# Kernel optimization log

Measured on AMD Instinct MI355X. Metric: run time of the kernel, lower is better.

## Reference

```python
import jax, jax.numpy as jnp
import numpy as np

EMBED = 1024
HEADS = 16

def setup_inputs() -> dict:
    key = jax.random.key(0)
    k1, k2, k3, k4, k5 = jax.random.split(key, 5)
    x = jax.random.normal(k1, (2, 2048, EMBED), dtype=jnp.float32)
    s = 1.0 / np.sqrt(EMBED)
    W_atten = jax.random.normal(k2, (EMBED, 3 * EMBED), dtype=jnp.float32) * s
    b_atten = jax.random.normal(k3, (3 * EMBED,), dtype=jnp.float32) * 0.01
    W_proj = jax.random.normal(k4, (EMBED, EMBED), dtype=jnp.float32) * s
    b_proj = jax.random.normal(k5, (EMBED,), dtype=jnp.float32) * 0.01
    return {"x": x, "W_atten": W_atten, "b_atten": b_atten, "W_proj": W_proj, "b_proj": b_proj}

def reference(x, W_atten, b_atten, W_proj, b_proj):
    B, T, C = x.shape
    H = HEADS
    hs = C // H
    qkv = x @ W_atten + b_atten  # [B,T,3C]
    # NOTE: original splits as k, q, v (k first)
    k, q, v = jnp.split(qkv, 3, axis=2)
    k = k.reshape(B, T, H, hs).transpose(0, 2, 1, 3)  # [B,H,T,hs]
    q = q.reshape(B, T, H, hs).transpose(0, 2, 1, 3)
    v = v.reshape(B, T, H, hs).transpose(0, 2, 1, 3)
    scores = jnp.einsum('bhqd,bhkd->bhqk', q, k) / jnp.sqrt(jnp.float32(hs))
    causal = jnp.tril(jnp.ones((T, T), dtype=bool))
    scores = jnp.where(causal[None, None, :, :], scores, jnp.float32(-jnp.inf))
    att = jax.nn.softmax(scores, axis=-1)
    out = jnp.einsum('bhqk,bhkd->bhqd', att, v)  # [B,H,T,hs]
    out = out.transpose(0, 2, 1, 3).reshape(B, T, C)
    return out @ W_proj + b_proj
```

## Files before the change

kernel.cpp:

```cpp
#include <hip/hip_runtime.h>

typedef unsigned short u16;
typedef unsigned int u32;
typedef __bf16 bf16;
typedef bf16 bf16x8 __attribute__((ext_vector_type(8)));
typedef float f32x4 __attribute__((ext_vector_type(4)));
typedef u32 u32x4 __attribute__((ext_vector_type(4)));
typedef u16 u16x4 __attribute__((ext_vector_type(4)));

#define EMBED 1024
#define HEADS 16
#define HS 64
#define BATCH 2
#define SEQ 2048
#define M_TOT (BATCH * SEQ)
#define N_QKV (3 * EMBED)
#define KDIM  EMBED

#define CSCALE 0.18033688011112042f
#define MREF (64.0f * CSCALE)

__device__ __forceinline__ u16 f2bf(float f) {
  u32 u = __builtin_bit_cast(u32, f);
  u32 r = u + 0x7fffu + ((u >> 16) & 1u);
  return (u16)(r >> 16);
}
__device__ __forceinline__ float bf2f(u16 h) {
  return __builtin_bit_cast(float, (u32)h << 16);
}
__device__ __forceinline__ bf16x8 frag16(const u16* p) {
  return __builtin_bit_cast(bf16x8, *(const u32x4*)p);
}
__device__ __forceinline__ bf16x8 frag16u(const u32* p) {
  return __builtin_bit_cast(bf16x8, *(const u32x4*)p);
}
__device__ __forceinline__ float cl(float v) {
  return fminf(fmaxf(v, -3.0e4f), 3.0e4f);
}
__device__ __forceinline__ u32 pk2bf(float lo, float hi) {
  const u32 ul = __builtin_bit_cast(u32, lo) + 0x8000u;
  const u32 uh = __builtin_bit_cast(u32, hi) + 0x8000u;
  return (ul >> 16) | (uh & 0xFFFF0000u);
}

typedef __attribute__((address_space(1))) void gvoid;
typedef __attribute__((address_space(3))) void lvoid;
__device__ __forceinline__ void glds16(const u16* g, u16* l) {
  __builtin_amdgcn_global_load_lds((gvoid*)g, (lvoid*)l, 16, 0, 0);
}

__global__ __launch_bounds__(256) void convert_kernel(
    const float* __restrict__ in, u16* __restrict__ out, int n4) {
  const int i = blockIdx.x * 256 + threadIdx.x;
  if (i < n4) {
    f32x4 v = *(const f32x4*)(in + (size_t)i * 4);
    u16x4 pk;
#pragma unroll
    for (int j = 0; j < 4; j++) pk[j] = f2bf(v[j]);
    *(u16x4*)(out + (size_t)i * 4) = pk;
  }
}

__global__ __launch_bounds__(256) void transpose_conv_kernel(
    const float* __restrict__ in, u16* __restrict__ out, int R, int C) {
  __shared__ u16 tile[32][33];
  const int c0 = blockIdx.x * 32;
  const int r0 = blockIdx.y * 32;
  const int tx = threadIdx.x;
  const int ty = threadIdx.y;
#pragma unroll
  for (int i = 0; i < 32; i += 8)
    tile[ty + i][tx] = f2bf(in[(size_t)(r0 + ty + i) * C + c0 + tx]);
  __syncthreads();
#pragma unroll
  for (int i = 0; i < 32; i += 8)
    out[(size_t)(c0 + ty + i) * R + r0 + tx] = tile[tx][ty + i];
}

__global__ __launch_bounds__(256) void gemm_qkv_kernel(
    const u16* __restrict__ A, const u16* __restrict__ wt,
    const u16* __restrict__ bias, u16* __restrict__ kq, u16* __restrict__ vt) {
  __shared__ u16 As[128 * 32];
  __shared__ u16 Bs[128 * 32];
  const int tid = threadIdx.x;
  const int lane = tid & 63;
  const int wave = tid >> 6;
  const int quad = lane >> 4;
  const int l16 = lane & 15;
  const int wr = wave >> 1;
  const int wc = wave & 1;
  const int m0 = blockIdx.y * 128;
  const int n0 = blockIdx.x * 128;

  f32x4 acc[4][4] = {};
  const int grow = tid >> 2;
  const int gcol = (tid & 3) * 8;

  for (int k0 = 0; k0 < KDIM; k0 += 32) {
    __syncthreads();
    glds16(A + (size_t)(m0 + grow) * KDIM + k0 + gcol, As + tid * 8);
    glds16(A + (size_t)(m0 + grow + 64) * KDIM + k0 + gcol, As + 2048 + tid * 8);
    glds16(wt + (size_t)(n0 + grow) * KDIM + k0 + gcol, Bs + tid * 8);
    glds16(wt + (size_t)(n0 + grow + 64) * KDIM + k0 + gcol, Bs + 2048 + tid * 8);
    __syncthreads();

    bf16x8 af[4], bfr[4];
#pragma unroll
    for (int i = 0; i < 4; i++) {
      af[i]  = frag16(As + (wr * 64 + i * 16 + l16) * 32 + quad * 8);
      bfr[i] = frag16(Bs + (wc * 64 + i * 16 + l16) * 32 + quad * 8);
    }
#pragma unroll
    for (int mi = 0; mi < 4; mi++)
#pragma unroll
      for (int ni = 0; ni < 4; ni++)
        acc[mi][ni] = __builtin_amdgcn_mfma_f32_16x16x32_bf16(
            af[mi], bfr[ni], acc[mi][ni], 0, 0, 0);
  }

#pragma unroll
  for (int ni = 0; ni < 4; ni++) {
    const int n = n0 + wc * 64 + ni * 16 + l16;
    const float bv = bf2f(bias[n]);
    if (n < 2 * EMBED) {
#pragma unroll
      for (int mi = 0; mi < 4; mi++)
#pragma unroll
        for (int r = 0; r < 4; r++) {
          const int m = m0 + wr * 64 + mi * 16 + quad * 4 + r;
          kq[(size_t)m * 2048 + n] = f2bf(cl(acc[mi][ni][r] + bv));
        }
    } else {
      const int hd = n - 2 * EMBED;
      const int h2 = hd >> 6;
      const int dc2 = (hd >> 4) & 3;
#pragma unroll
      for (int mi = 0; mi < 4; mi++) {
        const int mbase = m0 + wr * 64 + mi * 16 + quad * 4;
        const int bqi = mbase >> 11;
        const int t0 = mbase & 2047;
        const int kt2 = t0 >> 6;
        const int kc2 = (t0 >> 5) & 1;
        const int qt2 = (t0 >> 3) & 3;
        const int e0 = t0 & 7;
        u16x4 pk;
#pragma unroll
        for (int r = 0; r < 4; r++) pk[r] = f2bf(cl(acc[mi][ni][r] + bv));
        const size_t idx =
            ((((size_t)(bqi * 16 + h2) * 32 + kt2) * 2 + kc2) * 4 + dc2) * 512 +
            (qt2 * 16 + l16) * 8 + e0;
        *(u16x4*)(vt + idx) = pk;
      }
    }
  }
}

__global__ __launch_bounds__(128) void gemm_proj_kernel(
    const u16* __restrict__ A, const u16* __restrict__ wt,
    const u16* __restrict__ bias, float* __restrict__ out) {
  __shared__ u16 As[128 * 32];
  __shared__ u16 Bs[64 * 32];
  const int tid = threadIdx.x;
  const int lane = tid & 63;
  const int wave = tid >> 6;
  const int quad = lane >> 4;
  const int l16 = lane & 15;
  const int m0 = blockIdx.y * 128;
  const int n0 = blockIdx.x * 64;

  f32x4 acc[4][4] = {};
  const int grow = tid >> 2;
  const int gcol = (tid & 3) * 8;

  for (int k0 = 0; k0 < KDIM; k0 += 32) {
    __syncthreads();
#pragma unroll
    for (int p = 0; p < 4; p++)
      glds16(A + (size_t)(m0 + p * 32 + grow) * KDIM + k0 + gcol,
             As + p * 1024 + tid * 8);
#pragma unroll
    for (int p = 0; p < 2; p++)
      glds16(wt + (size_t)(n0 + p * 32 + grow) * KDIM + k0 + gcol,
             Bs + p * 1024 + tid * 8);
    __syncthreads();

    bf16x8 af[4], bfr[4];
#pragma unroll
    for (int i = 0; i < 4; i++) {
      af[i]  = frag16(As + (wave * 64 + i * 16 + l16) * 32 + quad * 8);
      bfr[i] = frag16(Bs + (i * 16 + l16) * 32 + quad * 8);
    }
#pragma unroll
    for (int mi = 0; mi < 4; mi++)
#pragma unroll
      for (int ni = 0; ni < 4; ni++)
        acc[mi][ni] = __builtin_amdgcn_mfma_f32_16x16x32_bf16(
            af[mi], bfr[ni], acc[mi][ni], 0, 0, 0);
  }

#pragma unroll
  for (int ni = 0; ni < 4; ni++) {
    const int n = n0 + ni * 16 + l16;
    const float bv = bf2f(bias[n]);
#pragma unroll
    for (int mi = 0; mi < 4; mi++)
#pragma unroll
      for (int r = 0; r < 4; r++) {
        const int m = m0 + wave * 64 + mi * 16 + quad * 4 + r;
        out[(size_t)m * EMBED + n] = cl(acc[mi][ni][r] + bv);
      }
  }
}

__global__ __launch_bounds__(64) void attn_kernel(
    const u16* __restrict__ kq, const u16* __restrict__ vt,
    u16* __restrict__ att) {
  __shared__ u16 Ks[2][64 * 64];
  __shared__ u32 Ps32[2][16 * 32];

  const int tid = threadIdx.x;
  const int quad = (tid >> 4) & 3;
  const int l16 = tid & 15;

  const int bh = blockIdx.x;
  const int qt32 = 63 - (int)blockIdx.y;
  const int q0 = qt32 * 32;
  const int bq = bh >> 4;
  const int h = bh & 15;

  int qg[2];
  bf16x8 bq0[2], bq1[2];
#pragma unroll
  for (int g = 0; g < 2; g++) {
    qg[g] = q0 + g * 16 + l16;
    const size_t qrow = (size_t)(bq * SEQ + qg[g]) * 2048 + EMBED + h * HS;
    bq0[g] = frag16(kq + qrow + quad * 8);
    bq1[g] = frag16(kq + qrow + 32 + quad * 8);
  }

  const u16* kb = kq + (size_t)bq * SEQ * 2048 + h * HS;
  const u16* vb2 = vt + (size_t)(bq * 16 + h) * 32 * 4096;
  const int psw32 = (l16 & 7) << 2;

  const int sw = quad ^ (l16 & 7);

  float lsum[2] = {0.0f, 0.0f};
  f32x4 o[2][4] = {};

  const int nkt = (qt32 >> 1) + 1;
#pragma unroll
  for (int p = 0; p < 8; p++) {
    const int row = p * 8 + (tid >> 3);
    const int sgc = (tid & 7) ^ (row & 7);
    glds16(kb + (size_t)row * 2048 + sgc * 8, Ks[0] + row * 64 + (tid & 7) * 8);
  }

  for (int kt = 0; kt < nkt; kt++) {
    const int k0 = kt * 64;
    __syncthreads();
    if (kt + 1 < nkt) {
      const int kn = k0 + 64;
      u16* dst = Ks[(kt + 1) & 1];
#pragma unroll
      for (int p = 0; p < 8; p++) {
        const int row = p * 8 + (tid >> 3);
        const int sgc = (tid & 7) ^ (row & 7);
        glds16(kb + (size_t)(kn + row) * 2048 + sgc * 8, dst + row * 64 + (tid & 7) * 8);
      }
    }
    const u16* KsB = Ks[kt & 1];

    bf16x8 va[2][4];
#pragma unroll
    for (int kc = 0; kc < 2; kc++)
#pragma unroll
      for (int dc = 0; dc < 4; dc++)
        va[kc][dc] = frag16(vb2 + (size_t)kt * 4096 +
                            ((kc * 4 + dc) * 64 + quad * 16 + l16) * 8);

    f32x4 st[2][4] = {};
    __builtin_amdgcn_s_setprio(1);
#pragma unroll
    for (int sub = 0; sub < 4; sub++) {
      const u16* kr = KsB + (sub * 16 + l16) * 64;
      const bf16x8 ka0 = frag16(kr + sw * 8);
      const bf16x8 ka1 = frag16(kr + (sw ^ 4) * 8);
#pragma unroll
      for (int g = 0; g < 2; g++) {
        st[g][sub] = __builtin_amdgcn_mfma_f32_16x16x32_bf16(
            ka0, bq0[g], st[g][sub], 0, 0, 0);
        st[g][sub] = __builtin_amdgcn_mfma_f32_16x16x32_bf16(
            ka1, bq1[g], st[g][sub], 0, 0, 0);
      }
    }
    __builtin_amdgcn_s_setprio(0);

    const bool diag = (kt == nkt - 1);
#pragma unroll
    for (int g = 0; g < 2; g++) {
      float p[4][4];
      if (diag) {
#pragma unroll
        for (int sub = 0; sub < 4; sub++)
#pragma unroll
          for (int r = 0; r < 4; r++) {
            const int key = k0 + sub * 16 + quad * 4 + r;
            const float e = __builtin_amdgcn_exp2f(st[g][sub][r] * CSCALE - MREF);
            p[sub][r] = (key <= qg[g]) ? e : 0.0f;
            lsum[g] += p[sub][r];
          }
      } else {
#pragma unroll
        for (int sub = 0; sub < 4; sub++)
#pragma unroll
          for (int r = 0; r < 4; r++) {
            p[sub][r] = __builtin_amdgcn_exp2f(st[g][sub][r] * CSCALE - MREF);
            lsum[g] += p[sub][r];
          }
      }
      u32* pw = Ps32[g];
#pragma unroll
      for (int sub = 0; sub < 4; sub++)
#pragma unroll
        for (int rp = 0; rp < 2; rp++)
          pw[l16 * 32 + ((sub * 8 + quad * 2 + rp) ^ psw32)] =
              pk2bf(p[sub][2 * rp], p[sub][2 * rp + 1]);
    }

#pragma unroll
    for (int g = 0; g < 2; g++) {
      u32* pw = Ps32[g];
#pragma unroll
      for (int kc = 0; kc < 2; kc++) {
        bf16x8 pb = frag16u(pw + l16 * 32 + ((kc * 16 + quad * 4) ^ psw32));
        __builtin_amdgcn_s_setprio(1);
#pragma unroll
        for (int dc = 0; dc < 4; dc++)
          o[g][dc] = __builtin_amdgcn_mfma_f32_16x16x32_bf16(
              va[kc][dc], pb, o[g][dc], 0, 0, 0);
        __builtin_amdgcn_s_setprio(0);
      }
    }
  }

#pragma unroll
  for (int g = 0; g < 2; g++) {
    float ls = lsum[g];
    ls += __shfl_xor(ls, 16);
    ls += __shfl_xor(ls, 32);
    const float inv = 1.0f / ls;
    const size_t obase = (size_t)(bq * SEQ + qg[g]) * EMBED + h * HS;
#pragma unroll
    for (int dc = 0; dc < 4; dc++) {
      u16 sv[4];
#pragma unroll
      for (int r = 0; r < 4; r++) sv[r] = f2bf(cl(o[g][dc][r] * inv));
      *(u32*)(att + obase + dc * 16 + quad * 4) = (u32)sv[0] | ((u32)sv[1] << 16);
      *(u32*)(att + obase + dc * 16 + quad * 4 + 2) = (u32)sv[2] | ((u32)sv[3] << 16);
    }
  }
}

extern "C" void kernel_launch(void* const* d_in, const int* in_sizes, int n_in,
                              void* d_out, int out_size, void* d_ws,
                              size_t ws_size, hipStream_t stream) {
  const float* x       = (const float*)d_in[0];
  const float* W_atten = (const float*)d_in[1];
  const float* b_atten = (const float*)d_in[2];
  const float* W_proj  = (const float*)d_in[3];
  const float* b_proj  = (const float*)d_in[4];

  u16* wt_a = (u16*)d_ws;
  u16* wt_p = wt_a + (size_t)N_QKV * EMBED;
  u16* ba   = wt_p + (size_t)EMBED * EMBED;
  u16* bp   = ba + N_QKV;
  u16* xb   = bp + EMBED;
  u16* kq   = xb + (size_t)M_TOT * KDIM;
  u16* vt   = kq + (size_t)M_TOT * 2048;
  u16* attb = xb;

  convert_kernel<<<(M_TOT * KDIM / 4 + 255) / 256, 256, 0, stream>>>(
      x, xb, M_TOT * KDIM / 4);
  convert_kernel<<<(N_QKV / 4 + 255) / 256, 256, 0, stream>>>(b_atten, ba, N_QKV / 4);
  convert_kernel<<<(EMBED / 4 + 255) / 256, 256, 0, stream>>>(b_proj, bp, EMBED / 4);
  transpose_conv_kernel<<<dim3(N_QKV / 32, EMBED / 32), dim3(32, 8), 0, stream>>>(
      W_atten, wt_a, EMBED, N_QKV);
  transpose_conv_kernel<<<dim3(EMBED / 32, EMBED / 32), dim3(32, 8), 0, stream>>>(
      W_proj, wt_p, EMBED, EMBED);
  gemm_qkv_kernel<<<dim3(N_QKV / 128, M_TOT / 128), 256, 0, stream>>>(
      xb, wt_a, ba, kq, vt);
  attn_kernel<<<dim3(BATCH * HEADS, SEQ / 32), 64, 0, stream>>>(kq, vt, attb);
  gemm_proj_kernel<<<dim3(EMBED / 64, M_TOT / 128), 128, 0, stream>>>(
      attb, wt_p, bp, (float*)d_out);
}
```

Measured before the change: 191.3 us.

## Pair causal query tiles per block and compute row sums via MFMA

The attention kernel now runs two independent waves per block. One wave takes a long causal query tile and the other a short one (yy and 63-yy), so every block gets the same amount of work and the grid is halved. Each wave has its own K and P shared buffers and waits on vmcnt instead of a block barrier. The softmax denominator, previously summed per element with shuffles, now comes from an extra MFMA of P against a ones vector. This adds shared memory per block and one MFMA per chunk, and drops the scalar adds and cross-lane reductions.

```diff
diff --git a/kernel.cpp b/kernel.cpp
--- a/kernel.cpp
+++ b/kernel.cpp
@@ -212,18 +212,21 @@
   }
 }
 
-__global__ __launch_bounds__(64) void attn_kernel(
+__global__ __launch_bounds__(128) void attn_kernel(
     const u16* __restrict__ kq, const u16* __restrict__ vt,
     u16* __restrict__ att) {
-  __shared__ u16 Ks[2][64 * 64];
-  __shared__ u32 Ps32[2][16 * 32];
+  __shared__ u16 Ks[2][2][64 * 64];
+  __shared__ u32 Ps32[2][2][16 * 32];
 
   const int tid = threadIdx.x;
-  const int quad = (tid >> 4) & 3;
-  const int l16 = tid & 15;
+  const int lane = tid & 63;
+  const int wave = tid >> 6;
+  const int quad = (lane >> 4) & 3;
+  const int l16 = lane & 15;
 
   const int bh = blockIdx.x;
-  const int qt32 = 63 - (int)blockIdx.y;
+  const int yy = (int)blockIdx.y;
+  const int qt32 = wave ? yy : (63 - yy);
   const int q0 = qt32 * 32;
   const int bq = bh >> 4;
   const int h = bh & 15;
@@ -241,34 +244,40 @@
   const u16* kb = kq + (size_t)bq * SEQ * 2048 + h * HS;
   const u16* vb2 = vt + (size_t)(bq * 16 + h) * 32 * 4096;
   const int psw32 = (l16 & 7) << 2;
-
   const int sw = quad ^ (l16 & 7);
 
-  float lsum[2] = {0.0f, 0.0f};
+  u32x4 onesu;
+#pragma unroll
+  for (int j = 0; j < 4; j++) onesu[j] = 0x3F803F80u;
+  const bf16x8 ones8 = __builtin_bit_cast(bf16x8, onesu);
+
   f32x4 o[2][4] = {};
+  f32x4 o4[2] = {};
 
   const int nkt = (qt32 >> 1) + 1;
+  u16* ksw = (u16*)Ks[wave];
+
 #pragma unroll
   for (int p = 0; p < 8; p++) {
-    const int row = p * 8 + (tid >> 3);
-    const int sgc = (tid & 7) ^ (row & 7);
-    glds16(kb + (size_t)row * 2048 + sgc * 8, Ks[0] + row * 64 + (tid & 7) * 8);
+    const int row = p * 8 + (lane >> 3);
+    const int sgc = (lane & 7) ^ (row & 7);
+    glds16(kb + (size_t)row * 2048 + sgc * 8, ksw + row * 64 + (lane & 7) * 8);
   }
 
   for (int kt = 0; kt < nkt; kt++) {
     const int k0 = kt * 64;
-    __syncthreads();
+    asm volatile("s_waitcnt vmcnt(0)" ::: "memory");
     if (kt + 1 < nkt) {
       const int kn = k0 + 64;
-      u16* dst = Ks[(kt + 1) & 1];
+      u16* dst = ksw + ((kt + 1) & 1) * (64 * 64);
 #pragma unroll
       for (int p = 0; p < 8; p++) {
-        const int row = p * 8 + (tid >> 3);
-        const int sgc = (tid & 7) ^ (row & 7);
-        glds16(kb + (size_t)(kn + row) * 2048 + sgc * 8, dst + row * 64 + (tid & 7) * 8);
-      }
-    }
-    const u16* KsB = Ks[kt & 1];
+        const int row = p * 8 + (lane >> 3);
+        const int sgc = (lane & 7) ^ (row & 7);
+        glds16(kb + (size_t)(kn + row) * 2048 + sgc * 8, dst + row * 64 + (lane & 7) * 8);
+      }
+    }
+    const u16* KsB = ksw + (kt & 1) * (64 * 64);
 
     bf16x8 va[2][4];
 #pragma unroll
@@ -307,18 +316,15 @@
             const int key = k0 + sub * 16 + quad * 4 + r;
             const float e = __builtin_amdgcn_exp2f(st[g][sub][r] * CSCALE - MREF);
             p[sub][r] = (key <= qg[g]) ? e : 0.0f;
-            lsum[g] += p[sub][r];
           }
       } else {
 #pragma unroll
         for (int sub = 0; sub < 4; sub++)
 #pragma unroll
-          for (int r = 0; r < 4; r++) {
+          for (int r = 0; r < 4; r++)
             p[sub][r] = __builtin_amdgcn_exp2f(st[g][sub][r] * CSCALE - MREF);
-            lsum[g] += p[sub][r];
-          }
-      }
-      u32* pw = Ps32[g];
+      }
+      u32* pw = Ps32[wave][g];
 #pragma unroll
       for (int sub = 0; sub < 4; sub++)
 #pragma unroll
@@ -329,7 +335,7 @@
 
 #pragma unroll
     for (int g = 0; g < 2; g++) {
-      u32* pw = Ps32[g];
+      u32* pw = Ps32[wave][g];
 #pragma unroll
       for (int kc = 0; kc < 2; kc++) {
         bf16x8 pb = frag16u(pw + l16 * 32 + ((kc * 16 + quad * 4) ^ psw32));
@@ -338,6 +344,8 @@
         for (int dc = 0; dc < 4; dc++)
           o[g][dc] = __builtin_amdgcn_mfma_f32_16x16x32_bf16(
               va[kc][dc], pb, o[g][dc], 0, 0, 0);
+        o4[g] = __builtin_amdgcn_mfma_f32_16x16x32_bf16(
+            ones8, pb, o4[g], 0, 0, 0);
         __builtin_amdgcn_s_setprio(0);
       }
     }
@@ -345,10 +353,7 @@
 
 #pragma unroll
   for (int g = 0; g < 2; g++) {
-    float ls = lsum[g];
-    ls += __shfl_xor(ls, 16);
-    ls += __shfl_xor(ls, 32);
-    const float inv = 1.0f / ls;
+    const float inv = 1.0f / o4[g][0];
     const size_t obase = (size_t)(bq * SEQ + qg[g]) * EMBED + h * HS;
 #pragma unroll
     for (int dc = 0; dc < 4; dc++) {
@@ -389,7 +394,7 @@
       W_proj, wt_p, EMBED, EMBED);
   gemm_qkv_kernel<<<dim3(N_QKV / 128, M_TOT / 128), 256, 0, stream>>>(
       xb, wt_a, ba, kq, vt);
-  attn_kernel<<<dim3(BATCH * HEADS, SEQ / 32), 64, 0, stream>>>(kq, vt, attb);
+  attn_kernel<<<dim3(BATCH * HEADS, SEQ / 64), 128, 0, stream>>>(kq, vt, attb);
   gemm_proj_kernel<<<dim3(EMBED / 64, M_TOT / 128), 128, 0, stream>>>(
       attb, wt_p, bp, (float*)d_out);
 }
```

Measured after the change: 196.4 us (median of 2 runs). 2.7% more time.
